# Optimization experiments

Measured on AMD Instinct MI355X. Metric: run time of the kernel, lower is better.

## Reference

```python
import jax, jax.numpy as jnp
import numpy as np

N_HEADS = 16
D_HEAD = 64
D_MODEL = 1024
WINDOW = 256
B, T = 4, 2048


def rotate_half(x):
    x1, x2 = jnp.split(x, 2, axis=-1)
    return jnp.concatenate([-x2, x1], axis=-1)


def apply_rope(x, cos, sin):
    return x * cos + rotate_half(x) * sin


def setup_inputs() -> dict:
    key = jax.random.key(0)
    ks = jax.random.split(key, 5)
    x = jax.random.normal(ks[0], (B, T, D_MODEL), dtype=jnp.float32)
    cos = jax.random.normal(ks[1], (1, T, 1, D_HEAD), dtype=jnp.float32)
    sin = jax.random.normal(ks[2], (1, T, 1, D_HEAD), dtype=jnp.float32)
    qkv_w = jax.random.normal(ks[3], (3 * D_MODEL, D_MODEL), dtype=jnp.float32) * (D_MODEL ** -0.5)
    out_w = jax.random.normal(ks[4], (D_MODEL, D_MODEL), dtype=jnp.float32) * (D_MODEL ** -0.5)
    return {"x": x, "cos": cos, "sin": sin, "qkv_w": qkv_w, "out_w": out_w}


def reference(x, cos, sin, qkv_w, out_w):
    Bc, Tc, C = x.shape
    # QKV projection (bias-free Linear: y = x @ W^T)
    qkv = jnp.einsum('btc,fc->btf', x, qkv_w)
    q, k, v = jnp.split(qkv, 3, axis=-1)
    # [B, H, T, d]
    def to_heads(t):
        return t.reshape(Bc, Tc, N_HEADS, D_HEAD).transpose(0, 2, 1, 3)
    q, k, v = to_heads(q), to_heads(k), to_heads(v)
    # RoPE: cos/sin [1, T, 1, d] -> [1, 1, T, d] broadcasting over heads
    cos_t = cos[:, :Tc].transpose(0, 2, 1, 3)
    sin_t = sin[:, :Tc].transpose(0, 2, 1, 3)
    q = apply_rope(q, cos_t, sin_t)
    k = apply_rope(k, cos_t, sin_t)
    # banded causal mask: allow j <= i and j >= i - (window-1)
    i = jnp.arange(Tc)[:, None]
    j = jnp.arange(Tc)[None, :]
    allowed = (j <= i) & (j >= i - (WINDOW - 1))  # [T, T]
    scale = 1.0 / jnp.sqrt(jnp.asarray(D_HEAD, dtype=q.dtype))
    scores = jnp.einsum('bhqd,bhkd->bhqk', q, k) * scale
    scores = jnp.where(allowed[None, None], scores, jnp.finfo(scores.dtype).min)
    attn = jax.nn.softmax(scores, axis=-1)
    out = jnp.einsum('bhqk,bhkd->bhqd', attn, v)
    out = out.transpose(0, 2, 1, 3).reshape(Bc, Tc, C)
    return jnp.einsum('btc,oc->bto', out, out_w)
```

## Files before the change

### kernel.cpp

```cpp
#include <hip/hip_runtime.h>

typedef __bf16 bf16_t;
typedef __bf16 bf16x8 __attribute__((ext_vector_type(8)));
typedef __bf16 bf16x4 __attribute__((ext_vector_type(4)));
typedef float f32x4 __attribute__((ext_vector_type(4)));

#define GLOAD_LDS16(gptr, lptr)                                                              \
  __builtin_amdgcn_global_load_lds((const __attribute__((address_space(1))) void*)(gptr),    \
                                   (__attribute__((address_space(3))) void*)(lptr), 16, 0, 0)

__device__ __forceinline__ f32x4 f32x4_zero() {
  f32x4 v; v[0] = 0.f; v[1] = 0.f; v[2] = 0.f; v[3] = 0.f; return v;
}

__device__ __forceinline__ int kxr(int r) { return (r & 7) ^ (((r >> 3) & 3) << 1); }

__device__ __forceinline__ void rope8(const bf16x8 xl, const bf16x8 xh,
                                      const float* __restrict__ cosb,
                                      const float* __restrict__ sinb, float sc,
                                      bf16x8& ol, bf16x8& oh) {
  float4 cl0 = *(const float4*)(cosb);
  float4 cl1 = *(const float4*)(cosb + 4);
  float4 ch0 = *(const float4*)(cosb + 32);
  float4 ch1 = *(const float4*)(cosb + 36);
  float4 sl0 = *(const float4*)(sinb);
  float4 sl1 = *(const float4*)(sinb + 4);
  float4 sh0 = *(const float4*)(sinb + 32);
  float4 sh1 = *(const float4*)(sinb + 36);
  float cl[8] = {cl0.x, cl0.y, cl0.z, cl0.w, cl1.x, cl1.y, cl1.z, cl1.w};
  float ch[8] = {ch0.x, ch0.y, ch0.z, ch0.w, ch1.x, ch1.y, ch1.z, ch1.w};
  float sl[8] = {sl0.x, sl0.y, sl0.z, sl0.w, sl1.x, sl1.y, sl1.z, sl1.w};
  float sh[8] = {sh0.x, sh0.y, sh0.z, sh0.w, sh1.x, sh1.y, sh1.z, sh1.w};
#pragma unroll
  for (int e = 0; e < 8; e++) {
    float a = (float)xl[e], b = (float)xh[e];
    ol[e] = (bf16_t)((a * cl[e] - b * sl[e]) * sc);
    oh[e] = (bf16_t)((b * ch[e] + a * sh[e]) * sc);
  }
}

__global__ void cast3_kernel(const float* __restrict__ a, const float* __restrict__ b,
                             const float* __restrict__ c, bf16_t* __restrict__ oa,
                             bf16_t* __restrict__ ob, bf16_t* __restrict__ oc) {
  int i = blockIdx.x * blockDim.x + threadIdx.x;
  const float* src; bf16_t* dst; int j;
  if (i < 2097152) { src = a; dst = oa; j = i; }
  else if (i < 2883584) { src = b; dst = ob; j = i - 2097152; }
  else { src = c; dst = oc; j = i - 2883584; }
  float4 v = ((const float4*)src)[j];
  bf16x4 o;
  o[0] = (bf16_t)v.x; o[1] = (bf16_t)v.y; o[2] = (bf16_t)v.z; o[3] = (bf16_t)v.w;
  ((bf16x4*)dst)[j] = o;
}

__global__ __launch_bounds__(256) void rope_k_kernel(bf16_t* __restrict__ kh,
                                                     const float* __restrict__ cosp,
                                                     const float* __restrict__ sinp) {
  int idx = blockIdx.x * 256 + threadIdx.x;
  int qo = idx & 3;
  int row = idx >> 2;
  int t = row & 2047;
  bf16x8* base = (bf16x8*)(kh + (size_t)row * 64);
  bf16x8 lo = base[qo], hi = base[qo + 4];
  bf16x8 ol, oh;
  rope8(lo, hi, cosp + t * 64 + qo * 8, sinp + t * 64 + qo * 8, 1.0f, ol, oh);
  base[qo] = ol;
  base[qo + 4] = oh;
}

template <int MODE>
__global__ __launch_bounds__(256) void gemm_bt_kernel(
    const bf16_t* __restrict__ A, const bf16_t* __restrict__ B, float* __restrict__ C,
    bf16_t* __restrict__ oq, bf16_t* __restrict__ ok_, bf16_t* __restrict__ ov,
    int M, int N, int K) {
  constexpr int BM = 128, BN = 128, BK = 32;
  __shared__ bf16_t As[BM * BK];
  __shared__ bf16_t Bs[BN * BK];
  const int tid = threadIdx.x;
  const int lane = tid & 63;
  const int wid = tid >> 6;
  const int wm = (wid >> 1) * 64;
  const int wn = (wid & 1) * 64;
  const int l16 = lane & 15;
  const int qd = lane >> 4;
  const int bm = blockIdx.x, bn = blockIdx.y;

  const int srow = tid >> 2;
  const int skol = (tid & 3) * 8;

  const bf16_t* gA = A + (size_t)(bm * BM + srow) * K + skol;
  const bf16_t* gB = B + (size_t)(bn * BN + srow) * K + skol;
  bf16_t* lA = &As[srow * BK + skol];
  bf16_t* lB = &Bs[srow * BK + skol];

  f32x4 acc[4][4];
#pragma unroll
  for (int mb = 0; mb < 4; mb++)
#pragma unroll
    for (int nb = 0; nb < 4; nb++) acc[mb][nb] = f32x4_zero();

  for (int k0 = 0; k0 < K; k0 += BK) {
    __syncthreads();
    GLOAD_LDS16(gA + k0, lA);
    GLOAD_LDS16(gA + (size_t)64 * K + k0, lA + 64 * BK);
    GLOAD_LDS16(gB + k0, lB);
    GLOAD_LDS16(gB + (size_t)64 * K + k0, lB + 64 * BK);
    __syncthreads();

    bf16x8 af[4], bfr[4];
#pragma unroll
    for (int mb = 0; mb < 4; mb++)
      af[mb] = *(const bf16x8*)&As[(wm + mb * 16 + l16) * BK + qd * 8];
#pragma unroll
    for (int nb = 0; nb < 4; nb++)
      bfr[nb] = *(const bf16x8*)&Bs[(wn + nb * 16 + l16) * BK + qd * 8];
#pragma unroll
    for (int mb = 0; mb < 4; mb++)
#pragma unroll
      for (int nb = 0; nb < 4; nb++)
        acc[mb][nb] = __builtin_amdgcn_mfma_f32_16x16x32_bf16(af[mb], bfr[nb], acc[mb][nb], 0, 0, 0);
  }

  if (MODE == 0) {
#pragma unroll
    for (int mb = 0; mb < 4; mb++)
#pragma unroll
      for (int nb = 0; nb < 4; nb++)
#pragma unroll
        for (int r = 0; r < 4; r++) {
          int row = bm * BM + wm + mb * 16 + qd * 4 + r;
          int col = bn * BN + wn + nb * 16 + l16;
          C[(size_t)row * N + col] = acc[mb][nb][r];
        }
  } else {
    const int part = bn >> 3;
    const int h = ((bn * 128 + wn) & 1023) >> 6;
    bf16_t* dst = (part == 0) ? oq : (part == 1) ? ok_ : ov;
#pragma unroll
    for (int mb = 0; mb < 4; mb++)
#pragma unroll
      for (int r = 0; r < 4; r++) {
        int row = bm * BM + wm + mb * 16 + qd * 4 + r;
        int b = row >> 11, t = row & 2047;
        size_t basei = (((size_t)(b * 16 + h)) * 2048 + t) * 64;
#pragma unroll
        for (int nb = 0; nb < 4; nb++)
          dst[basei + nb * 16 + l16] = (bf16_t)acc[mb][nb][r];
      }
  }
}

__global__ __launch_bounds__(256) void attn_kernel(
    const bf16_t* __restrict__ qh, const bf16_t* __restrict__ kh,
    const bf16_t* __restrict__ vh, bf16_t* __restrict__ ao,
    const float* __restrict__ cosp, const float* __restrict__ sinp) {
  __shared__ bf16_t qs[64 * 64];
  __shared__ bf16_t ks[64 * 64];
  __shared__ bf16_t vs[64 * 64];
  __shared__ bf16_t vswz[8 * 64 * 8];
  __shared__ bf16_t ps[4][16 * 64];

  const int tid = threadIdx.x;
  const int lane = tid & 63;
  const int wid = tid >> 6;
  const int l16 = lane & 15;
  const int qd = lane >> 4;

  const int bh = blockIdx.x;
  const int i0 = blockIdx.y * 64;
  const int b = bh >> 4, h = bh & 15;

  auto swz4 = [](int f) { int r = f >> 3; return r * 8 + ((f & 7) ^ (r & 7)); };
  const int r0 = tid >> 3, q0 = tid & 7;
  const int rr = tid >> 2, qo = tid & 3;

  {
    const bf16x8* src = (const bf16x8*)(qh + ((size_t)bh * 2048 + i0) * 64);
    bf16x8* dst = (bf16x8*)qs;
    const int fl = rr * 8 + qo, fh = fl + 4;
    bf16x8 ol, oh;
    rope8(src[fl], src[fh], cosp + (i0 + rr) * 64 + qo * 8, sinp + (i0 + rr) * 64 + qo * 8,
          0.18033688011112042f, ol, oh);
    dst[swz4(fl)] = ol;
    dst[swz4(fh)] = oh;
  }

  bf16x8 bones;
#pragma unroll
  for (int e = 0; e < 8; e++) bones[e] = (bf16_t)1.0f;

  float l_i[4] = {0.f, 0.f, 0.f, 0.f};
  f32x4 oacc[4];
#pragma unroll
  for (int nb = 0; nb < 4; nb++) oacc[nb] = f32x4_zero();

  const int c1 = i0 >> 6;
  const int c0 = (c1 >= 4) ? (c1 - 4) : 0;
  const size_t bhbase = (size_t)bh * 2048;

  uint4 kr0, kr1, vr0, vr1;
  {
    const uint4* ksrc = (const uint4*)(kh + (bhbase + (size_t)c0 * 64) * 64);
    const uint4* vsrc = (const uint4*)(vh + (bhbase + (size_t)c0 * 64) * 64);
    kr0 = ksrc[tid]; kr1 = ksrc[tid + 256];
    vr0 = vsrc[tid]; vr1 = vsrc[tid + 256];
  }

  for (int c = c0; c <= c1; c++) {
    const int j0 = c * 64;
    __syncthreads();
    {
      uint4* kdst = (uint4*)ks;
      uint4* vdst = (uint4*)vs;
      kdst[swz4(tid)] = kr0;
      kdst[swz4(tid + 256)] = kr1;
      vdst[r0 * 8 + (q0 ^ kxr(r0))] = vr0;
      vdst[(r0 + 32) * 8 + (q0 ^ kxr(r0 + 32))] = vr1;
    }
    if (c < c1) {
      const uint4* ksrc = (const uint4*)(kh + (bhbase + (size_t)(c + 1) * 64) * 64);
      const uint4* vsrc = (const uint4*)(vh + (bhbase + (size_t)(c + 1) * 64) * 64);
      kr0 = ksrc[tid]; kr1 = ksrc[tid + 256];
      vr0 = vsrc[tid]; vr1 = vsrc[tid + 256];
    }
    __syncthreads();

    f32x4 sacc[4];
#pragma unroll
    for (int nb = 0; nb < 4; nb++) sacc[nb] = f32x4_zero();
#pragma unroll
    for (int kk = 0; kk < 2; kk++) {
      bf16x8 afr = *(const bf16x8*)&qs[(wid * 16 + l16) * 64 + (((kk * 4 + qd) ^ (l16 & 7)) * 8)];
#pragma unroll
      for (int nb = 0; nb < 4; nb++) {
        bf16x8 bfr = *(const bf16x8*)&ks[(nb * 16 + l16) * 64 + (((kk * 4 + qd) ^ (l16 & 7)) * 8)];
        sacc[nb] = __builtin_amdgcn_mfma_f32_16x16x32_bf16(afr, bfr, sacc[nb], 0, 0, 0);
      }
    }

#pragma unroll
    for (int p2 = 0; p2 < 2; p2++) {
      int combo = p2 * 4 + wid;
      int jbase = (combo >> 2) * 32 + (lane >> 4) * 8;
      int dcol = (combo & 3) * 16 + (lane & 15);
      int bb = dcol >> 3, dlo = dcol & 7;
      bf16x8 v8;
#pragma unroll
      for (int e = 0; e < 8; e++) {
        int row = jbase + e;
        v8[e] = vs[row * 64 + ((bb ^ kxr(row)) * 8) + dlo];
      }
      *(bf16x8*)&vswz[(combo * 64 + lane) * 8] = v8;
    }

#pragma unroll
    for (int r = 0; r < 4; r++) {
      const int i = i0 + wid * 16 + qd * 4 + r;
      const int prow = qd * 4 + r;
#pragma unroll
      for (int nb = 0; nb < 4; nb++) {
        const int j = j0 + nb * 16 + l16;
        bool valid = (j <= i) && (j + 256 > i);
        float p = valid ? exp2f(sacc[nb][r]) : 0.f;
        ps[wid][prow * 64 + (((nb * 2 + (l16 >> 3)) ^ (prow & 7)) * 8) + (l16 & 7)] = (bf16_t)p;
      }
    }

    __syncthreads();

    f32x4 lacc = f32x4_zero();
#pragma unroll
    for (int kk = 0; kk < 2; kk++) {
      bf16x8 afr = *(const bf16x8*)&ps[wid][l16 * 64 + (((kk * 4 + qd) ^ (l16 & 7)) * 8)];
      lacc = __builtin_amdgcn_mfma_f32_16x16x32_bf16(afr, bones, lacc, 0, 0, 0);
#pragma unroll
      for (int nb = 0; nb < 4; nb++) {
        bf16x8 bfr = *(const bf16x8*)&vswz[((kk * 4 + nb) * 64 + lane) * 8];
        oacc[nb] = __builtin_amdgcn_mfma_f32_16x16x32_bf16(afr, bfr, oacc[nb], 0, 0, 0);
      }
    }
#pragma unroll
    for (int r = 0; r < 4; r++) l_i[r] += lacc[r];
  }

#pragma unroll
  for (int nb = 0; nb < 4; nb++) {
#pragma unroll
    for (int r = 0; r < 4; r++) {
      int t = i0 + wid * 16 + qd * 4 + r;
      ao[((size_t)(b * 2048 + t)) * 1024 + h * 64 + nb * 16 + l16] =
          (bf16_t)(oacc[nb][r] / l_i[r]);
    }
  }
}

extern "C" void kernel_launch(void* const* d_in, const int* in_sizes, int n_in,
                              void* d_out, int out_size, void* d_ws, size_t ws_size,
                              hipStream_t stream) {
  const float* x    = (const float*)d_in[0];
  const float* cosp = (const float*)d_in[1];
  const float* sinp = (const float*)d_in[2];
  const float* qkvw = (const float*)d_in[3];
  const float* outw = (const float*)d_in[4];
  float* out = (float*)d_out;

  char* ws = (char*)d_ws;
  bf16_t* xb  = (bf16_t*)(ws + 0);
  bf16_t* qwb = (bf16_t*)(ws + 16777216);
  bf16_t* owb = (bf16_t*)(ws + 23068672);
  bf16_t* qhp = (bf16_t*)(ws + 25165824);
  bf16_t* khp = (bf16_t*)(ws + 41943040);
  bf16_t* vhp = (bf16_t*)(ws + 58720256);
  bf16_t* aop = (bf16_t*)(ws + 75497472);

  cast3_kernel<<<12288, 256, 0, stream>>>(x, qkvw, outw, xb, qwb, owb);

  gemm_bt_kernel<1><<<dim3(64, 24), 256, 0, stream>>>(xb, qwb, nullptr, qhp, khp, vhp,
                                                      8192, 3072, 1024);
  rope_k_kernel<<<2048, 256, 0, stream>>>(khp, cosp, sinp);
  attn_kernel<<<dim3(64, 32), 256, 0, stream>>>(qhp, khp, vhp, aop, cosp, sinp);
  gemm_bt_kernel<0><<<dim3(64, 8), 256, 0, stream>>>(aop, owb, out, nullptr, nullptr, nullptr,
                                                     8192, 1024, 1024);
}
```

Before: 241.3 us.

## Triple-buffer GEMM with async LDS loads, larger tiles and XOR swizzle

Rewrites the shared GEMM kernel used for the QKV and output projections. Tiles grow to 256x128 with BK=64 and 512 threads (8 waves). A three-stage LDS ring is prefetched two tiles ahead through global_load_lds, with vmcnt waits and a single barrier per iteration. An XOR swizzle on the LDS layout avoids bank conflicts, and s_setprio is raised around the MFMA block. The aim is to hide global memory latency and cut synchronisation overhead, at the cost of about 144KB of LDS per block (one block per CU) and fewer blocks in the grid.

```diff
diff --git a/kernel.cpp b/kernel.cpp
--- a/kernel.cpp
+++ b/kernel.cpp
@@ -68,84 +68,129 @@
   base[qo + 4] = oh;
 }
 
+#define GT_AELE 16384
+#define GT_BELE 8192
+#define GT_TILE (GT_AELE + GT_BELE)
+
+__device__ __forceinline__ void gt_stage(const bf16_t* __restrict__ A,
+                                         const bf16_t* __restrict__ B, bf16_t* buf,
+                                         int bm, int bn, int t, int K, int tid) {
+#pragma unroll
+  for (int i = 0; i < 4; i++) {
+    int gi = tid + i * 512;
+    int row = gi >> 3, g = gi & 7;
+    const bf16_t* src = A + (size_t)(bm * 256 + row) * K + t * 64 + ((g ^ (row & 7)) << 3);
+    GLOAD_LDS16(src, buf + gi * 8);
+  }
+#pragma unroll
+  for (int i = 0; i < 2; i++) {
+    int gi = tid + i * 512;
+    int row = gi >> 3, g = gi & 7;
+    const bf16_t* src = B + (size_t)(bn * 128 + row) * K + t * 64 + ((g ^ (row & 7)) << 3);
+    GLOAD_LDS16(src, buf + GT_AELE + gi * 8);
+  }
+}
+
 template <int MODE>
-__global__ __launch_bounds__(256) void gemm_bt_kernel(
+__global__ __launch_bounds__(512, 1) void gemm_bt_kernel(
     const bf16_t* __restrict__ A, const bf16_t* __restrict__ B, float* __restrict__ C,
     bf16_t* __restrict__ oq, bf16_t* __restrict__ ok_, bf16_t* __restrict__ ov,
     int M, int N, int K) {
-  constexpr int BM = 128, BN = 128, BK = 32;
-  __shared__ bf16_t As[BM * BK];
-  __shared__ bf16_t Bs[BN * BK];
+  __shared__ bf16_t lds[3 * GT_TILE];
+
   const int tid = threadIdx.x;
   const int lane = tid & 63;
   const int wid = tid >> 6;
-  const int wm = (wid >> 1) * 64;
-  const int wn = (wid & 1) * 64;
+  const int wr = wid >> 1;
+  const int wc = wid & 1;
   const int l16 = lane & 15;
   const int qd = lane >> 4;
   const int bm = blockIdx.x, bn = blockIdx.y;
 
-  const int srow = tid >> 2;
-  const int skol = (tid & 3) * 8;
-
-  const bf16_t* gA = A + (size_t)(bm * BM + srow) * K + skol;
-  const bf16_t* gB = B + (size_t)(bn * BN + srow) * K + skol;
-  bf16_t* lA = &As[srow * BK + skol];
-  bf16_t* lB = &Bs[srow * BK + skol];
-
   f32x4 acc[4][4];
 #pragma unroll
-  for (int mb = 0; mb < 4; mb++)
-#pragma unroll
-    for (int nb = 0; nb < 4; nb++) acc[mb][nb] = f32x4_zero();
-
-  for (int k0 = 0; k0 < K; k0 += BK) {
-    __syncthreads();
-    GLOAD_LDS16(gA + k0, lA);
-    GLOAD_LDS16(gA + (size_t)64 * K + k0, lA + 64 * BK);
-    GLOAD_LDS16(gB + k0, lB);
-    GLOAD_LDS16(gB + (size_t)64 * K + k0, lB + 64 * BK);
-    __syncthreads();
-
-    bf16x8 af[4], bfr[4];
-#pragma unroll
-    for (int mb = 0; mb < 4; mb++)
-      af[mb] = *(const bf16x8*)&As[(wm + mb * 16 + l16) * BK + qd * 8];
-#pragma unroll
-    for (int nb = 0; nb < 4; nb++)
-      bfr[nb] = *(const bf16x8*)&Bs[(wn + nb * 16 + l16) * BK + qd * 8];
-#pragma unroll
-    for (int mb = 0; mb < 4; mb++)
-#pragma unroll
-      for (int nb = 0; nb < 4; nb++)
-        acc[mb][nb] = __builtin_amdgcn_mfma_f32_16x16x32_bf16(af[mb], bfr[nb], acc[mb][nb], 0, 0, 0);
+  for (int m = 0; m < 4; m++)
+#pragma unroll
+    for (int n = 0; n < 4; n++) acc[m][n] = f32x4_zero();
+
+  const int NT = K >> 6;
+
+  gt_stage(A, B, lds, bm, bn, 0, K, tid);
+  gt_stage(A, B, lds + GT_TILE, bm, bn, 1, K, tid);
+  asm volatile("s_waitcnt vmcnt(6)" ::: "memory");
+  __builtin_amdgcn_s_barrier();
+  __builtin_amdgcn_sched_barrier(0);
+
+  int s = 0;
+  for (int j = 0; j < NT; ++j) {
+    if (j + 2 < NT) {
+      int s2 = s + 2; if (s2 >= 3) s2 -= 3;
+      gt_stage(A, B, lds + s2 * GT_TILE, bm, bn, j + 2, K, tid);
+    }
+
+    const bf16_t* bufc = lds + s * GT_TILE;
+    bf16x8 af[4][2], bf[4][2];
+#pragma unroll
+    for (int m = 0; m < 4; m++)
+#pragma unroll
+      for (int kk = 0; kk < 2; kk++) {
+        int row = wr * 64 + m * 16 + l16;
+        af[m][kk] = *(const bf16x8*)&bufc[row * 64 + (((kk * 4 + qd) ^ (row & 7)) << 3)];
+      }
+#pragma unroll
+    for (int n = 0; n < 4; n++)
+#pragma unroll
+      for (int kk = 0; kk < 2; kk++) {
+        int row = wc * 64 + n * 16 + l16;
+        bf[n][kk] = *(const bf16x8*)&bufc[GT_AELE + row * 64 + (((kk * 4 + qd) ^ (row & 7)) << 3)];
+      }
+
+    __builtin_amdgcn_s_setprio(1);
+#pragma unroll
+    for (int m = 0; m < 4; m++)
+#pragma unroll
+      for (int n = 0; n < 4; n++)
+#pragma unroll
+        for (int kk = 0; kk < 2; kk++)
+          acc[m][n] = __builtin_amdgcn_mfma_f32_16x16x32_bf16(af[m][kk], bf[n][kk], acc[m][n], 0, 0, 0);
+    __builtin_amdgcn_s_setprio(0);
+
+    if (j + 2 < NT) {
+      asm volatile("s_waitcnt vmcnt(6)" ::: "memory");
+    } else {
+      asm volatile("s_waitcnt vmcnt(0)" ::: "memory");
+    }
+    __builtin_amdgcn_s_barrier();
+    __builtin_amdgcn_sched_barrier(0);
+    s = (s == 2) ? 0 : s + 1;
   }
 
   if (MODE == 0) {
 #pragma unroll
-    for (int mb = 0; mb < 4; mb++)
-#pragma unroll
-      for (int nb = 0; nb < 4; nb++)
+    for (int m = 0; m < 4; m++)
+#pragma unroll
+      for (int n = 0; n < 4; n++)
 #pragma unroll
         for (int r = 0; r < 4; r++) {
-          int row = bm * BM + wm + mb * 16 + qd * 4 + r;
-          int col = bn * BN + wn + nb * 16 + l16;
-          C[(size_t)row * N + col] = acc[mb][nb][r];
+          int row = bm * 256 + wr * 64 + m * 16 + qd * 4 + r;
+          int col = bn * 128 + wc * 64 + n * 16 + l16;
+          C[(size_t)row * N + col] = acc[m][n][r];
         }
   } else {
-    const int part = bn >> 3;
-    const int h = ((bn * 128 + wn) & 1023) >> 6;
+    const int colbase = bn * 128 + wc * 64;
+    const int part = colbase >> 10;
+    const int h = (colbase & 1023) >> 6;
     bf16_t* dst = (part == 0) ? oq : (part == 1) ? ok_ : ov;
 #pragma unroll
-    for (int mb = 0; mb < 4; mb++)
+    for (int m = 0; m < 4; m++)
 #pragma unroll
       for (int r = 0; r < 4; r++) {
-        int row = bm * BM + wm + mb * 16 + qd * 4 + r;
+        int row = bm * 256 + wr * 64 + m * 16 + qd * 4 + r;
         int b = row >> 11, t = row & 2047;
         size_t basei = (((size_t)(b * 16 + h)) * 2048 + t) * 64;
 #pragma unroll
-        for (int nb = 0; nb < 4; nb++)
-          dst[basei + nb * 16 + l16] = (bf16_t)acc[mb][nb][r];
+        for (int n = 0; n < 4; n++)
+          dst[basei + n * 16 + l16] = (bf16_t)acc[m][n][r];
       }
   }
 }
@@ -315,10 +360,10 @@
 
   cast3_kernel<<<12288, 256, 0, stream>>>(x, qkvw, outw, xb, qwb, owb);
 
-  gemm_bt_kernel<1><<<dim3(64, 24), 256, 0, stream>>>(xb, qwb, nullptr, qhp, khp, vhp,
+  gemm_bt_kernel<1><<<dim3(32, 24), 512, 0, stream>>>(xb, qwb, nullptr, qhp, khp, vhp,
                                                       8192, 3072, 1024);
   rope_k_kernel<<<2048, 256, 0, stream>>>(khp, cosp, sinp);
   attn_kernel<<<dim3(64, 32), 256, 0, stream>>>(qhp, khp, vhp, aop, cosp, sinp);
-  gemm_bt_kernel<0><<<dim3(64, 8), 256, 0, stream>>>(aop, owb, out, nullptr, nullptr, nullptr,
+  gemm_bt_kernel<0><<<dim3(32, 8), 512, 0, stream>>>(aop, owb, out, nullptr, nullptr, nullptr,
                                                      8192, 1024, 1024);
 }
```

Measured after the change: 224.0 us. 1.08x faster.
